# Performance work log

Measured on AMD Instinct MI355X. Metric: run time of the kernel, lower is better.

The kernel has to match this reference:

```python
import jax, jax.numpy as jnp
import numpy as np

DIM = 128
B, LQ, LK = 8, 2048, 2048


def setup_inputs() -> dict:
    key = jax.random.key(0)
    k1, k2, k3 = jax.random.split(key, 3)
    output = jax.random.normal(k1, (B, LQ, DIM), dtype=jnp.float32)
    context = jax.random.normal(k2, (B, LK, DIM), dtype=jnp.float32)
    mask = jax.random.randint(k3, (B, LQ, LK), 0, 2).astype(jnp.bool_)
    return {"output": output, "context": context, "mask": mask}


def reference(output, context, mask):
    temperature = jnp.asarray(np.power(DIM, 0.5), dtype=output.dtype)
    # scores: [B, Lq, Lk]
    attn = jnp.einsum('bqd,bkd->bqk', output, context) / temperature
    attn = jnp.where(mask, -jnp.inf, attn)
    out_attn = jax.nn.log_softmax(attn, axis=-1)
    p = jax.nn.softmax(attn, axis=-1)
    # dropout is identity in eval/reference mode
    out = jnp.einsum('bqk,bkd->bqd', p, context)
    return (out, out_attn)
```

## Files before the change

### kernel.cpp

```cpp
#include <hip/hip_runtime.h>
#include <cstdint>


#define DIMV 128
constexpr int BB = 8;
constexpr int LQ = 2048;
constexpr int LK = 2048;
constexpr float RTEMP = 0.08838834764831843f;

typedef _Float16 half8 __attribute__((ext_vector_type(8)));
typedef _Float16 half4v __attribute__((ext_vector_type(4)));
typedef float float4v __attribute__((ext_vector_type(4)));

__global__ __launch_bounds__(256) void prep_kernel(const float* __restrict__ q,
                                                   const float* __restrict__ ctx,
                                                   _Float16* __restrict__ Qf,
                                                   _Float16* __restrict__ Kf,
                                                   _Float16* __restrict__ Vf) {
    __shared__ float tile[32][132];
    const int tid  = threadIdx.x;
    const int mode = blockIdx.x >> 9;
    const int t    = blockIdx.x & 511;
    const int b    = t >> 6;
    const int r0   = (t & 63) * 32;
    const float4* s4 = (const float4*)((mode == 0 ? q : ctx) + ((size_t)b * 2048 + r0) * DIMV);
    for (int v = 0; v < 4; v++) {
        int off = tid + v * 256;
        float4 f = s4[off];
        int row = off >> 5, c4 = (off & 31) * 4;
        tile[row][c4 + 0] = f.x; tile[row][c4 + 1] = f.y;
        tile[row][c4 + 2] = f.z; tile[row][c4 + 3] = f.w;
    }
    __syncthreads();
    if (mode < 2) {
        _Float16* dst = (mode == 0 ? Qf : Kf) + (size_t)b * (2048 * DIMV);
        for (int c = 0; c < 2; c++) {
            int chunk = tid + c * 256;
            int t2 = chunk >> 8, kk = (chunk >> 6) & 3, lane = chunk & 63;
            int quad = lane >> 4, l16 = lane & 15;
            int r = t2 * 16 + l16, d0 = kk * 32 + quad * 8;
            half8 h;
            for (int e = 0; e < 8; e++) h[e] = (_Float16)tile[r][d0 + e];
            size_t tl = (size_t)(r0 >> 4) + t2;
            *(half8*)(dst + ((tl * 4 + kk) * 64 + lane) * 8) = h;
        }
    } else {
        _Float16* dst = Vf + (size_t)b * (2048 * DIMV);
        size_t i = r0 >> 5;
        for (int c = 0; c < 2; c++) {
            int chunk = tid + c * 256;
            int dt = chunk >> 6, lane = chunk & 63;
            int quad = lane >> 4, l16 = lane & 15;
            half8 h;
            for (int e = 0; e < 8; e++) h[e] = (_Float16)tile[quad * 8 + e][dt * 16 + l16];
            *(half8*)(dst + ((i * 8 + dt) * 64 + lane) * 8) = h;
        }
    }
}

__global__ __launch_bounds__(256, 2)
void attn_kernel(const unsigned char* __restrict__ mask,
                 const _Float16* __restrict__ Qf, const _Float16* __restrict__ Kf,
                 const _Float16* __restrict__ Vf,
                 float* __restrict__ out, float* __restrict__ out_attn) {
    constexpr int TQ = 16;
    constexpr int SSTR = 2052;
    __shared__ __attribute__((aligned(16))) _Float16 S[TQ * SSTR];
    __shared__ float redm[4][TQ];
    __shared__ float mfin[TQ];

    const int tid  = threadIdx.x;
    const int wave = tid >> 6;
    const int lane = tid & 63;
    const int l16  = lane & 15;
    const int quad = lane >> 4;

    const int b  = blockIdx.x & 7;
    const int q0 = (blockIdx.x >> 3) * TQ;
    const int qt = blockIdx.x >> 3;

    const _Float16* Qb = Qf + (size_t)b * (2048 * DIMV);
    const _Float16* Kb = Kf + (size_t)b * (2048 * DIMV);
    const _Float16* Vb = Vf + (size_t)b * (2048 * DIMV);

    half8 afrag[4];
    for (int kk = 0; kk < 4; kk++)
        afrag[kk] = *(const half8*)(Qb + (((size_t)qt * 4 + kk) * 64 + lane) * 8);

    float mloc[4];
    for (int r = 0; r < 4; r++) mloc[r] = -__builtin_inff();

    for (int ct = 0; ct < 32; ct++) {
        const int cT = wave * 32 + ct;
        const _Float16* kp = Kb + (size_t)cT * 4 * 64 * 8;
        float4v acc = (float4v){0.f, 0.f, 0.f, 0.f};
        for (int kk = 0; kk < 4; kk++) {
            half8 bf = *(const half8*)(kp + (kk * 64 + lane) * 8);
            acc = __builtin_amdgcn_mfma_f32_16x16x32_f16(afrag[kk], bf, acc, 0, 0, 0);
        }
        for (int r = 0; r < 4; r++) {
            float v = acc[r] * RTEMP;
            mloc[r] = fmaxf(mloc[r], v);
            S[(quad * 4 + r) * SSTR + cT * 16 + l16] = (_Float16)v;
        }
    }
    for (int r = 0; r < 4; r++) {
        float v = mloc[r];
        v = fmaxf(v, __shfl_xor(v, 1));
        v = fmaxf(v, __shfl_xor(v, 2));
        v = fmaxf(v, __shfl_xor(v, 4));
        v = fmaxf(v, __shfl_xor(v, 8));
        mloc[r] = v;
    }
    if (l16 == 0)
        for (int r = 0; r < 4; r++)
            redm[wave][quad * 4 + r] = mloc[r];
    __syncthreads();
    if (tid < TQ)
        mfin[tid] = fmaxf(fmaxf(redm[0][tid], redm[1][tid]), fmaxf(redm[2][tid], redm[3][tid]));
    __syncthreads();

    {
        const int row = tid >> 4;
        const int j   = tid & 15;
        const float m = mfin[row];
        const unsigned char* mrow = mask + ((size_t)b * LQ + q0 + row) * LK;
        _Float16* srow = S + row * SSTR;
        const float NEGINF = -__builtin_inff();
        float lsum = 0.f;
        for (int i = 0; i < 32; i++) {
            const int col = i * 64 + j * 4;
            half4v sv = *(half4v*)(srow + col);
            uint32_t mv = *(const uint32_t*)(mrow + col);
            for (int u = 0; u < 4; u++) {
                float s = (float)sv[u];
                if ((mv >> (8 * u)) & 0xffu) { s = NEGINF; sv[u] = (_Float16)NEGINF; }
                lsum += __expf(s - m);
            }
            *(half4v*)(srow + col) = sv;
        }
        lsum += __shfl_xor(lsum, 1);
        lsum += __shfl_xor(lsum, 2);
        lsum += __shfl_xor(lsum, 4);
        lsum += __shfl_xor(lsum, 8);
        const float logl = __logf(lsum);

        float* oa_row = out_attn + ((size_t)b * LQ + q0 + row) * LK;
        for (int i = 0; i < 32; i++) {
            const int col = i * 64 + j * 4;
            half4v sv = *(half4v*)(srow + col);
            half4v pv;
            float lp[4];
            for (int u = 0; u < 4; u++) {
                float s = (float)sv[u];
                float logp = s - m - logl;
                logp = fmaxf(logp, -1.0e30f);
                lp[u] = logp;
                pv[u] = (_Float16)__expf(logp);
            }
            float4 f = {lp[0], lp[1], lp[2], lp[3]};
            *(float4*)(oa_row + col) = f;
            *(half4v*)(srow + col) = pv;
        }
    }
    __syncthreads();

    float4v oacc[2];
    for (int ct = 0; ct < 2; ct++) oacc[ct] = (float4v){0.f, 0.f, 0.f, 0.f};
    for (int i = 0; i < 64; i++) {
        half8 pa = *(half8*)(S + (size_t)l16 * SSTR + i * 32 + quad * 8);
        for (int ct = 0; ct < 2; ct++) {
            const int dt = wave * 2 + ct;
            half8 bf = *(const half8*)(Vb + (((size_t)i * 8 + dt) * 64 + lane) * 8);
            oacc[ct] = __builtin_amdgcn_mfma_f32_16x16x32_f16(pa, bf, oacc[ct], 0, 0, 0);
        }
    }
    for (int ct = 0; ct < 2; ct++)
        for (int r = 0; r < 4; r++)
            out[((size_t)b * LQ + q0 + quad * 4 + r) * DIMV + wave * 32 + ct * 16 + l16] = oacc[ct][r];
}

extern "C" void kernel_launch(void* const* d_in, const int* in_sizes, int n_in,
                              void* d_out, int out_size, void* d_ws, size_t ws_size,
                              hipStream_t stream) {
    const float* q_f32 = (const float*)d_in[0];
    const float* c_f32 = (const float*)d_in[1];
    const unsigned char* mask = (const unsigned char*)d_in[2];

    float* out      = (float*)d_out;
    float* out_attn = out + (size_t)BB * LQ * DIMV;

    _Float16* Qf = (_Float16*)d_ws;
    _Float16* Kf = Qf + (size_t)BB * LQ * DIMV;
    _Float16* Vf = Kf + (size_t)BB * LK * DIMV;

    prep_kernel<<<1536, 256, 0, stream>>>(q_f32, c_f32, Qf, Kf, Vf);
    attn_kernel<<<BB * (LQ / 16), 256, 0, stream>>>(mask, Qf, Kf, Vf, out, out_attn);
}
```

Before: 287.5 us.

## Recompute scores in two passes and bit-pack the mask instead of staging scores in LDS

The mask is packed into 32-bit bitfields in extra prep blocks. The attention kernel no longer stores the full 16x2048 fp16 score tile in shared memory. It computes QK^T twice: the first pass gathers exp sums without subtracting a max, and the second writes log-probabilities and feeds P through a small per-wave scratch into the PV MFMAs. Partial outputs are merged with LDS atomics. This cuts LDS use so occupancy can rise from 2 to 4 blocks per CU, at the cost of doubling the QK matmul and dropping the max subtraction, which risks overflow for large scores.

```diff
diff --git a/kernel.cpp b/kernel.cpp
--- a/kernel.cpp
+++ b/kernel.cpp
@@ -9,16 +9,39 @@
 constexpr float RTEMP = 0.08838834764831843f;
 
 typedef _Float16 half8 __attribute__((ext_vector_type(8)));
-typedef _Float16 half4v __attribute__((ext_vector_type(4)));
 typedef float float4v __attribute__((ext_vector_type(4)));
 
 __global__ __launch_bounds__(256) void prep_kernel(const float* __restrict__ q,
                                                    const float* __restrict__ ctx,
+                                                   const unsigned char* __restrict__ mask,
                                                    _Float16* __restrict__ Qf,
                                                    _Float16* __restrict__ Kf,
-                                                   _Float16* __restrict__ Vf) {
+                                                   _Float16* __restrict__ Vf,
+                                                   uint32_t* __restrict__ pm) {
+    const int tid = threadIdx.x;
+    if (blockIdx.x >= 1536) {
+        const int mb = blockIdx.x - 1536;
+        const int g  = mb * 8 + (tid >> 5);
+        const int w0 = (tid & 31) * 2;
+        const uint4* p = (const uint4*)(mask + (size_t)g * 2048 + w0 * 32);
+        uint32_t* dst = pm + (size_t)g * 64 + w0;
+        for (int wi = 0; wi < 2; wi++) {
+            uint32_t bits = 0;
+            for (int h = 0; h < 2; h++) {
+                uint4 v = p[wi * 2 + h];
+                uint32_t d[4] = {v.x, v.y, v.z, v.w};
+                for (int k = 0; k < 4; k++) {
+                    uint32_t x = d[k];
+                    x |= x >> 4; x |= x >> 2; x |= x >> 1;
+                    x &= 0x01010101u;
+                    bits |= ((x * 0x01020408u) >> 24 & 0xF) << (h * 16 + k * 4);
+                }
+            }
+            dst[wi] = bits;
+        }
+        return;
+    }
     __shared__ float tile[32][132];
-    const int tid  = threadIdx.x;
     const int mode = blockIdx.x >> 9;
     const int t    = blockIdx.x & 511;
     const int b    = t >> 6;
@@ -49,25 +72,25 @@
         size_t i = r0 >> 5;
         for (int c = 0; c < 2; c++) {
             int chunk = tid + c * 256;
-            int dt = chunk >> 6, lane = chunk & 63;
+            int nt = chunk >> 6, lane = chunk & 63;
             int quad = lane >> 4, l16 = lane & 15;
             half8 h;
-            for (int e = 0; e < 8; e++) h[e] = (_Float16)tile[quad * 8 + e][dt * 16 + l16];
-            *(half8*)(dst + ((i * 8 + dt) * 64 + lane) * 8) = h;
+            for (int e = 0; e < 8; e++) h[e] = (_Float16)tile[quad * 8 + e][nt * 16 + l16];
+            *(half8*)(dst + ((i * 8 + nt) * 64 + lane) * 8) = h;
         }
     }
 }
 
-__global__ __launch_bounds__(256, 2)
-void attn_kernel(const unsigned char* __restrict__ mask,
+__global__ __launch_bounds__(256, 4)
+void attn_kernel(const uint32_t* __restrict__ pm,
                  const _Float16* __restrict__ Qf, const _Float16* __restrict__ Kf,
                  const _Float16* __restrict__ Vf,
                  float* __restrict__ out, float* __restrict__ out_attn) {
-    constexpr int TQ = 16;
-    constexpr int SSTR = 2052;
-    __shared__ __attribute__((aligned(16))) _Float16 S[TQ * SSTR];
-    __shared__ float redm[4][TQ];
-    __shared__ float mfin[TQ];
+    constexpr int PSTR = 40;
+    __shared__ float sumbuf[4][16];
+    __shared__ float loglbuf[16];
+    __shared__ float obuf[16][128];
+    __shared__ __attribute__((aligned(16))) _Float16 pscr[4][16 * PSTR];
 
     const int tid  = threadIdx.x;
     const int wave = tid >> 6;
@@ -76,108 +99,118 @@
     const int quad = lane >> 4;
 
     const int b  = blockIdx.x & 7;
-    const int q0 = (blockIdx.x >> 3) * TQ;
     const int qt = blockIdx.x >> 3;
+    const int q0 = qt * 16;
 
     const _Float16* Qb = Qf + (size_t)b * (2048 * DIMV);
     const _Float16* Kb = Kf + (size_t)b * (2048 * DIMV);
     const _Float16* Vb = Vf + (size_t)b * (2048 * DIMV);
+    const uint32_t* pmb = pm + ((size_t)b * 2048 + q0) * 64;
+
+    for (int i = tid; i < 16 * 128; i += 256) ((float*)obuf)[i] = 0.f;
 
     half8 afrag[4];
+#pragma unroll
     for (int kk = 0; kk < 4; kk++)
         afrag[kk] = *(const half8*)(Qb + (((size_t)qt * 4 + kk) * 64 + lane) * 8);
 
-    float mloc[4];
-    for (int r = 0; r < 4; r++) mloc[r] = -__builtin_inff();
-
-    for (int ct = 0; ct < 32; ct++) {
-        const int cT = wave * 32 + ct;
-        const _Float16* kp = Kb + (size_t)cT * 4 * 64 * 8;
-        float4v acc = (float4v){0.f, 0.f, 0.f, 0.f};
-        for (int kk = 0; kk < 4; kk++) {
-            half8 bf = *(const half8*)(kp + (kk * 64 + lane) * 8);
-            acc = __builtin_amdgcn_mfma_f32_16x16x32_f16(afrag[kk], bf, acc, 0, 0, 0);
-        }
-        for (int r = 0; r < 4; r++) {
-            float v = acc[r] * RTEMP;
-            mloc[r] = fmaxf(mloc[r], v);
-            S[(quad * 4 + r) * SSTR + cT * 16 + l16] = (_Float16)v;
-        }
-    }
+    float lsum[4] = {0.f, 0.f, 0.f, 0.f};
+    for (int ch = 0; ch < 16; ch++) {
+        const int w = wave * 16 + ch;
+        uint32_t mw[4];
+#pragma unroll
+        for (int r = 0; r < 4; r++)
+            mw[r] = pmb[(size_t)(quad * 4 + r) * 64 + w];
+#pragma unroll
+        for (int h = 0; h < 2; h++) {
+            const int cT = w * 2 + h;
+            const _Float16* kp = Kb + (size_t)cT * 2048;
+            float4v acc = (float4v){0.f, 0.f, 0.f, 0.f};
+#pragma unroll
+            for (int kk = 0; kk < 4; kk++) {
+                half8 bf = *(const half8*)(kp + (kk * 64 + lane) * 8);
+                acc = __builtin_amdgcn_mfma_f32_16x16x32_f16(afrag[kk], bf, acc, 0, 0, 0);
+            }
+            const int bitpos = h * 16 + l16;
+#pragma unroll
+            for (int r = 0; r < 4; r++) {
+                float e = __expf(acc[r] * RTEMP);
+                lsum[r] += ((mw[r] >> bitpos) & 1u) ? 0.f : e;
+            }
+        }
+    }
+#pragma unroll
     for (int r = 0; r < 4; r++) {
-        float v = mloc[r];
-        v = fmaxf(v, __shfl_xor(v, 1));
-        v = fmaxf(v, __shfl_xor(v, 2));
-        v = fmaxf(v, __shfl_xor(v, 4));
-        v = fmaxf(v, __shfl_xor(v, 8));
-        mloc[r] = v;
+        float v = lsum[r];
+        v += __shfl_xor(v, 1);
+        v += __shfl_xor(v, 2);
+        v += __shfl_xor(v, 4);
+        v += __shfl_xor(v, 8);
+        lsum[r] = v;
     }
     if (l16 == 0)
-        for (int r = 0; r < 4; r++)
-            redm[wave][quad * 4 + r] = mloc[r];
-    __syncthreads();
-    if (tid < TQ)
-        mfin[tid] = fmaxf(fmaxf(redm[0][tid], redm[1][tid]), fmaxf(redm[2][tid], redm[3][tid]));
-    __syncthreads();
-
-    {
-        const int row = tid >> 4;
-        const int j   = tid & 15;
-        const float m = mfin[row];
-        const unsigned char* mrow = mask + ((size_t)b * LQ + q0 + row) * LK;
-        _Float16* srow = S + row * SSTR;
-        const float NEGINF = -__builtin_inff();
-        float lsum = 0.f;
-        for (int i = 0; i < 32; i++) {
-            const int col = i * 64 + j * 4;
-            half4v sv = *(half4v*)(srow + col);
-            uint32_t mv = *(const uint32_t*)(mrow + col);
-            for (int u = 0; u < 4; u++) {
-                float s = (float)sv[u];
-                if ((mv >> (8 * u)) & 0xffu) { s = NEGINF; sv[u] = (_Float16)NEGINF; }
-                lsum += __expf(s - m);
-            }
-            *(half4v*)(srow + col) = sv;
-        }
-        lsum += __shfl_xor(lsum, 1);
-        lsum += __shfl_xor(lsum, 2);
-        lsum += __shfl_xor(lsum, 4);
-        lsum += __shfl_xor(lsum, 8);
-        const float logl = __logf(lsum);
-
-        float* oa_row = out_attn + ((size_t)b * LQ + q0 + row) * LK;
-        for (int i = 0; i < 32; i++) {
-            const int col = i * 64 + j * 4;
-            half4v sv = *(half4v*)(srow + col);
-            half4v pv;
-            float lp[4];
-            for (int u = 0; u < 4; u++) {
-                float s = (float)sv[u];
-                float logp = s - m - logl;
-                logp = fmaxf(logp, -1.0e30f);
-                lp[u] = logp;
-                pv[u] = (_Float16)__expf(logp);
-            }
-            float4 f = {lp[0], lp[1], lp[2], lp[3]};
-            *(float4*)(oa_row + col) = f;
-            *(half4v*)(srow + col) = pv;
-        }
-    }
-    __syncthreads();
-
-    float4v oacc[2];
-    for (int ct = 0; ct < 2; ct++) oacc[ct] = (float4v){0.f, 0.f, 0.f, 0.f};
-    for (int i = 0; i < 64; i++) {
-        half8 pa = *(half8*)(S + (size_t)l16 * SSTR + i * 32 + quad * 8);
-        for (int ct = 0; ct < 2; ct++) {
-            const int dt = wave * 2 + ct;
-            half8 bf = *(const half8*)(Vb + (((size_t)i * 8 + dt) * 64 + lane) * 8);
-            oacc[ct] = __builtin_amdgcn_mfma_f32_16x16x32_f16(pa, bf, oacc[ct], 0, 0, 0);
-        }
-    }
-    for (int ct = 0; ct < 2; ct++)
-        for (int r = 0; r < 4; r++)
-            out[((size_t)b * LQ + q0 + quad * 4 + r) * DIMV + wave * 32 + ct * 16 + l16] = oacc[ct][r];
+#pragma unroll
+        for (int r = 0; r < 4; r++)
+            sumbuf[wave][quad * 4 + r] = lsum[r];
+    __syncthreads();
+    if (tid < 16)
+        loglbuf[tid] = __logf(sumbuf[0][tid] + sumbuf[1][tid] + sumbuf[2][tid] + sumbuf[3][tid]);
+    __syncthreads();
+    float logl[4];
+#pragma unroll
+    for (int r = 0; r < 4; r++) logl[r] = loglbuf[quad * 4 + r];
+
+    _Float16* myscr = &pscr[wave][0];
+    float4v oacc[8];
+#pragma unroll
+    for (int nt = 0; nt < 8; nt++) oacc[nt] = (float4v){0.f, 0.f, 0.f, 0.f};
+
+    for (int ch = 0; ch < 16; ch++) {
+        const int w = wave * 16 + ch;
+        uint32_t mw[4];
+#pragma unroll
+        for (int r = 0; r < 4; r++)
+            mw[r] = pmb[(size_t)(quad * 4 + r) * 64 + w];
+#pragma unroll
+        for (int h = 0; h < 2; h++) {
+            const int cT = w * 2 + h;
+            const _Float16* kp = Kb + (size_t)cT * 2048;
+            float4v acc = (float4v){0.f, 0.f, 0.f, 0.f};
+#pragma unroll
+            for (int kk = 0; kk < 4; kk++) {
+                half8 bf = *(const half8*)(kp + (kk * 64 + lane) * 8);
+                acc = __builtin_amdgcn_mfma_f32_16x16x32_f16(afrag[kk], bf, acc, 0, 0, 0);
+            }
+            const int bitpos = h * 16 + l16;
+#pragma unroll
+            for (int r = 0; r < 4; r++) {
+                float s = acc[r] * RTEMP;
+                bool masked = (mw[r] >> bitpos) & 1u;
+                float logp = masked ? -1.0e30f : (s - logl[r]);
+                out_attn[((size_t)b * 2048 + q0 + quad * 4 + r) * 2048 + cT * 16 + l16] = logp;
+                float p = masked ? 0.f : __expf(logp);
+                myscr[(quad * 4 + r) * PSTR + h * 16 + l16] = (_Float16)p;
+            }
+        }
+        half8 pa = *(half8*)(myscr + l16 * PSTR + quad * 8);
+        const int kidx = wave * 16 + ch;
+#pragma unroll
+        for (int nt = 0; nt < 8; nt++) {
+            half8 bf = *(const half8*)(Vb + (((size_t)kidx * 8 + nt) * 64 + lane) * 8);
+            oacc[nt] = __builtin_amdgcn_mfma_f32_16x16x32_f16(pa, bf, oacc[nt], 0, 0, 0);
+        }
+    }
+
+#pragma unroll
+    for (int nt = 0; nt < 8; nt++)
+#pragma unroll
+        for (int r = 0; r < 4; r++)
+            atomicAdd(&obuf[quad * 4 + r][nt * 16 + l16], oacc[nt][r]);
+    __syncthreads();
+    for (int i = tid; i < 16 * 128; i += 256) {
+        int row = i >> 7, col = i & 127;
+        out[((size_t)b * 2048 + q0 + row) * 128 + col] = obuf[row][col];
+    }
 }
 
 extern "C" void kernel_launch(void* const* d_in, const int* in_sizes, int n_in,
@@ -193,7 +226,8 @@
     _Float16* Qf = (_Float16*)d_ws;
     _Float16* Kf = Qf + (size_t)BB * LQ * DIMV;
     _Float16* Vf = Kf + (size_t)BB * LK * DIMV;
-
-    prep_kernel<<<1536, 256, 0, stream>>>(q_f32, c_f32, Qf, Kf, Vf);
-    attn_kernel<<<BB * (LQ / 16), 256, 0, stream>>>(mask, Qf, Kf, Vf, out, out_attn);
+    uint32_t* pm = (uint32_t*)(Vf + (size_t)BB * LK * DIMV);
+
+    prep_kernel<<<1536 + 2048, 256, 0, stream>>>(q_f32, c_f32, mask, Qf, Kf, Vf, pm);
+    attn_kernel<<<BB * (LQ / 16), 256, 0, stream>>>(pm, Qf, Kf, Vf, out, out_attn);
 }
```

Result: slower. 313.5 us (+9.1%).
